# Kernel tuning notes

Measured on AMD Instinct MI355X. Metric: run time of the kernel, lower is better.

The kernel has to match this reference:

```python
import jax, jax.numpy as jnp
import numpy as np

LQ, LK, B, E, H = 1024, 1024, 8, 1024, 16


def setup_inputs() -> dict:
    key0 = jax.random.key(0)
    ks = jax.random.split(key0, 6)
    std = float(np.sqrt(2.0 / (E + E)))
    query = jax.random.normal(ks[0], (LQ, B, E), dtype=jnp.float32)
    key = jax.random.normal(ks[1], (LK, B, E), dtype=jnp.float32)
    attn_mask = jax.random.randint(ks[2], (B, LK), 0, 2).astype(bool)
    in_proj_weight_q = std * jax.random.normal(ks[3], (E, E), dtype=jnp.float32)
    in_proj_weight_kv = std * jax.random.normal(ks[4], (2 * E, E), dtype=jnp.float32)
    out_proj_weight = std * jax.random.normal(ks[5], (E, E), dtype=jnp.float32)
    return {
        "query": query,
        "key": key,
        "attn_mask": attn_mask,
        "in_proj_weight_q": in_proj_weight_q,
        "in_proj_weight_kv": in_proj_weight_kv,
        "out_proj_weight": out_proj_weight,
        "num_heads": H,
    }


def reference(query, key, attn_mask, in_proj_weight_q, in_proj_weight_kv, out_proj_weight, num_heads):
    Lq, Bs, Em = query.shape
    Lk = key.shape[0]
    Hd = Em // num_heads  # head_dim
    scaling = Hd ** (-0.5)

    # input projections: F.linear(x, W) == x @ W.T  (no bias)
    q = jnp.einsum("lbe,fe->lbf", query, in_proj_weight_q) * scaling
    kv = jnp.einsum("lbe,fe->lbf", key, in_proj_weight_kv)
    k, v = jnp.split(kv, 2, axis=-1)

    # [len, b, e] -> [b, h, len, d]
    def to_heads(x, L):
        return x.reshape(L, Bs, num_heads, Hd).transpose(1, 2, 0, 3)

    qh = to_heads(q, Lq)
    kh = to_heads(k, Lk)
    vh = to_heads(v, Lk)

    scores = jnp.einsum("bhqd,bhkd->bhqk", qh, kh)  # [B,H,Lq,Lk]
    neg = jnp.asarray(-1e9, scores.dtype)
    scores = jnp.where(attn_mask[:, None, None, :], neg, scores)
    attn = jax.nn.softmax(scores, axis=-1)  # coverage (dropout=0, eval)

    ctx = jnp.einsum("bhqk,bhkd->bhqd", attn, vh)  # [B,H,Lq,d]
    ctx = ctx.transpose(2, 0, 1, 3).reshape(Lq, Bs, Em)
    out = jnp.einsum("lbe,fe->lbf", ctx, out_proj_weight)
    return out, attn
```

## Files before the change

### kernel.cpp

```cpp
#include <hip/hip_runtime.h>
#include <hip/hip_bf16.h>
#include <cstdint>
#include <cstddef>

constexpr int LQc = 1024, LKc = 1024, Bc = 8, Ec = 1024, Hc = 16, Dc = 64;

typedef __bf16 bf16;
typedef __bf16 bf16x4 __attribute__((ext_vector_type(4)));
typedef __bf16 bf16x8 __attribute__((ext_vector_type(8)));
typedef float  f32x4  __attribute__((ext_vector_type(4)));

#define MFMA16(a, b, c) __builtin_amdgcn_mfma_f32_16x16x32_bf16((a), (b), (c), 0, 0, 0)

__device__ __forceinline__ void gload_lds16(const bf16* g, bf16* l) {
  __builtin_amdgcn_global_load_lds((const __attribute__((address_space(1))) void*)g,
                                   (__attribute__((address_space(3))) void*)l, 16, 0, 0);
}

__global__ __launch_bounds__(256) void k_convert(const float* __restrict__ q,
                                                 const float* __restrict__ k,
                                                 const float* __restrict__ wq,
                                                 const float* __restrict__ wkv,
                                                 const float* __restrict__ wout,
                                                 bf16* __restrict__ dst) {
  const size_t i = ((size_t)blockIdx.x * 256 + threadIdx.x) * 8;
  const float* src; size_t off; float sc = 1.0f;
  if (i < 8388608)        { src = q;    off = i; sc = 0.125f; }
  else if (i < 16777216)  { src = k;    off = i - 8388608; }
  else if (i < 17825792)  { src = wq;   off = i - 16777216; }
  else if (i < 19922944)  { src = wkv;  off = i - 17825792; }
  else                    { src = wout; off = i - 19922944; }
  const f32x4 a = *reinterpret_cast<const f32x4*>(src + off);
  const f32x4 b = *reinterpret_cast<const f32x4*>(src + off + 4);
  bf16x8 o;
  o[0] = (bf16)(a.x * sc); o[1] = (bf16)(a.y * sc);
  o[2] = (bf16)(a.z * sc); o[3] = (bf16)(a.w * sc);
  o[4] = (bf16)(b.x * sc); o[5] = (bf16)(b.y * sc);
  o[6] = (bf16)(b.z * sc); o[7] = (bf16)(b.w * sc);
  *reinterpret_cast<bf16x8*>(dst + i) = o;
}

template <int MODE>
__global__ __launch_bounds__(256) void k_gemm(const bf16* __restrict__ Aq,
                                              const bf16* __restrict__ Ak,
                                              const bf16* __restrict__ Wq,
                                              const bf16* __restrict__ Wkv,
                                              bf16* __restrict__ qh,
                                              bf16* __restrict__ kh,
                                              bf16* __restrict__ vh,
                                              float* __restrict__ o_f) {
  __shared__ bf16 As[128 * 32];
  __shared__ bf16 Bs[128 * 32];

  const int tid  = threadIdx.x;
  const int lane = tid & 63, wave = tid >> 6;
  const int wm = wave & 1, wn = wave >> 1;

  const int cpx = gridDim.x >> 3;
  const int logical = (blockIdx.x & 7) * cpx + (blockIdx.x >> 3);
  const int bx = logical & 63, by = logical >> 6;
  const int m0 = bx * 128;

  const bf16* Ap;
  const bf16* Wp;
  bf16* Op = nullptr;
  if constexpr (MODE == 0) {
    if (by < 8)       { Ap = Aq; Wp = Wq  + (size_t)by * 131072;        Op = qh; }
    else if (by < 16) { Ap = Ak; Wp = Wkv + (size_t)(by - 8) * 131072;  Op = kh; }
    else              { Ap = Ak; Wp = Wkv + 1048576 + (size_t)(by - 16) * 131072; Op = vh; }
  } else {
    Ap = Aq; Wp = Wq + (size_t)by * 131072;
  }
  const int col0 = (by & 7) * 128;

  const int fr = lane & 15, fo = (lane >> 4) * 8;

  f32x4 acc[4][4] = {};

  const int srow = lane >> 2;
  const int scol = (lane & 3) * 8;
  const bf16* ga = Ap + (size_t)(m0 + wave * 32 + srow) * Ec + scol;
  const bf16* gb = Wp + (size_t)(wave * 32 + srow) * Ec + scol;
  bf16* lA = As + wave * 1024;
  bf16* lB = Bs + wave * 1024;

  for (int k0 = 0; k0 < Ec; k0 += 32) {
    gload_lds16(ga + k0, lA);
    gload_lds16(ga + k0 + 16 * Ec, lA + 512);
    gload_lds16(gb + k0, lB);
    gload_lds16(gb + k0 + 16 * Ec, lB + 512);
    __syncthreads();

    bf16x8 a[4], b[4];
#pragma unroll
    for (int i = 0; i < 4; ++i) {
      a[i] = *reinterpret_cast<const bf16x8*>(As + (wm * 64 + i * 16 + fr) * 32 + fo);
      b[i] = *reinterpret_cast<const bf16x8*>(Bs + (wn * 64 + i * 16 + fr) * 32 + fo);
    }
#pragma unroll
    for (int i = 0; i < 4; ++i)
#pragma unroll
      for (int j = 0; j < 4; ++j) acc[i][j] = MFMA16(a[i], b[j], acc[i][j]);
    __syncthreads();
  }

  const int rb = (lane >> 4) * 4;
#pragma unroll
  for (int i = 0; i < 4; ++i) {
#pragma unroll
    for (int j = 0; j < 4; ++j) {
      const int col = col0 + wn * 64 + j * 16 + fr;
#pragma unroll
      for (int r = 0; r < 4; ++r) {
        const int tok = m0 + wm * 64 + i * 16 + rb + r;
        const float val = acc[i][j][r];
        if constexpr (MODE == 0) {
          const int lq = tok >> 3, bb = tok & 7;
          const int h = col >> 6, dd = col & 63;
          Op[(((size_t)(bb * Hc + h)) * LQc + lq) * Dc + dd] = (bf16)val;
        } else {
          o_f[(size_t)tok * Ec + col] = val;
        }
      }
    }
  }
}

__global__ __launch_bounds__(256) void k_vtrans(const bf16* __restrict__ Vh,
                                                bf16* __restrict__ VhT) {
  __shared__ bf16 tile[64][72];
  const int bh = blockIdx.y;
  const int l0 = blockIdx.x * 64;
  const int r = threadIdx.x >> 3, c = (threadIdx.x & 7) * 8;
#pragma unroll
  for (int rr = 0; rr < 2; ++rr) {
    const int row = rr * 32 + r;
    *reinterpret_cast<bf16x8*>(&tile[row][c]) =
        *reinterpret_cast<const bf16x8*>(Vh + ((size_t)bh * LKc + l0 + row) * Dc + c);
  }
  __syncthreads();
#pragma unroll
  for (int rr = 0; rr < 2; ++rr) {
    const int d = rr * 32 + r;
    bf16x8 o;
#pragma unroll
    for (int j = 0; j < 8; ++j) o[j] = tile[c + j][d];
    *reinterpret_cast<bf16x8*>(VhT + ((size_t)bh * Dc + d) * LKc + l0 + c) = o;
  }
}

__global__ __launch_bounds__(256) void k_attn(const bf16* __restrict__ Qh,
                                              const bf16* __restrict__ Kh,
                                              const bf16* __restrict__ VhT,
                                              const int* __restrict__ mask,
                                              float* __restrict__ attn_out,
                                              bf16* __restrict__ ctx_out) {
  __shared__ bf16 sP[32][1032];
  __shared__ float smask[1024];
  __shared__ float psum[4][32];
  __shared__ float rinv[32];

  const int tid = threadIdx.x;
  const int lane = tid & 63, wave = tid >> 6;
  const bool pv_first = (blockIdx.x >> 9) & 1;

  int flat = blockIdx.x;
  flat = (flat & 7) * 512 + (flat >> 3);
  const int bh = flat >> 5;
  const int q0 = (flat & 31) * 32;
  const int b = bh >> 4, h = bh & 15;
  const int fr = lane & 15, fo = (lane >> 4) * 8, rb = (lane >> 4) * 4;

#pragma unroll
  for (int c = tid; c < 1024; c += 256)
    smask[c] = mask[b * LKc + c] ? -1e9f : 0.0f;

  bf16x8 qf[2][2];
  const bf16* Qb = Qh + ((size_t)bh * LQc + q0) * Dc;
#pragma unroll
  for (int m = 0; m < 2; ++m)
#pragma unroll
    for (int kc = 0; kc < 2; ++kc)
      qf[m][kc] = *reinterpret_cast<const bf16x8*>(Qb + (size_t)(m * 16 + fr) * Dc + kc * 32 + fo);
  __syncthreads();

  const bf16* Kb = Kh + (size_t)bh * LKc * Dc;
  float s0[4] = {0.f, 0.f, 0.f, 0.f}, s1[4] = {0.f, 0.f, 0.f, 0.f};
#pragma unroll 4
  for (int t = 0; t < 16; ++t) {
    const int n = (wave * 16 + t) * 16;
    const bf16* kp = Kb + (size_t)(n + fr) * Dc + fo;
    const bf16x8 kf0 = *reinterpret_cast<const bf16x8*>(kp);
    const bf16x8 kf1 = *reinterpret_cast<const bf16x8*>(kp + 32);
    f32x4 c0 = {}, c1 = {};
    c0 = MFMA16(qf[0][0], kf0, c0);
    c0 = MFMA16(qf[0][1], kf1, c0);
    c1 = MFMA16(qf[1][0], kf0, c1);
    c1 = MFMA16(qf[1][1], kf1, c1);
    const int col = n + fr;
    const float madd = smask[col];
#pragma unroll
    for (int r = 0; r < 4; ++r) {
      const float e0 = __expf(c0[r] + madd);
      const float e1 = __expf(c1[r] + madd);
      s0[r] += e0; s1[r] += e1;
      sP[rb + r][col]      = (bf16)e0;
      sP[16 + rb + r][col] = (bf16)e1;
    }
  }
#pragma unroll
  for (int o = 1; o < 16; o <<= 1)
#pragma unroll
    for (int r = 0; r < 4; ++r) {
      s0[r] += __shfl_xor(s0[r], o, 64);
      s1[r] += __shfl_xor(s1[r], o, 64);
    }
  if (fr == 0) {
#pragma unroll
    for (int r = 0; r < 4; ++r) {
      psum[wave][rb + r]      = s0[r];
      psum[wave][16 + rb + r] = s1[r];
    }
  }
  __syncthreads();
  if (tid < 32)
    rinv[tid] = 1.0f / (psum[0][tid] + psum[1][tid] + psum[2][tid] + psum[3][tid]);
  __syncthreads();

  float* ap = attn_out + ((size_t)bh * LQc + q0) * LKc;
  const bf16* Vb = VhT + ((size_t)bh * Dc + wave * 16 + fr) * LKc;
  f32x4 cacc0 = {}, cacc1 = {};

  if (!pv_first) {
#pragma unroll 4
    for (int r = 0; r < 32; ++r) {
      const float rs = rinv[r];
      const bf16x4 v = *reinterpret_cast<const bf16x4*>(&sP[r][tid * 4]);
      f32x4 p;
      p.x = (float)v.x * rs; p.y = (float)v.y * rs;
      p.z = (float)v.z * rs; p.w = (float)v.w * rs;
      __builtin_nontemporal_store(p, reinterpret_cast<f32x4*>(ap + (size_t)r * LKc + tid * 4));
    }
#pragma unroll 4
    for (int kc = 0; kc < 1024; kc += 32) {
      const bf16x8 vf  = *reinterpret_cast<const bf16x8*>(Vb + kc + fo);
      const bf16x8 pa0 = *reinterpret_cast<const bf16x8*>(&sP[fr][kc + fo]);
      const bf16x8 pa1 = *reinterpret_cast<const bf16x8*>(&sP[16 + fr][kc + fo]);
      cacc0 = MFMA16(pa0, vf, cacc0);
      cacc1 = MFMA16(pa1, vf, cacc1);
    }
  } else {
#pragma unroll 4
    for (int kc = 0; kc < 1024; kc += 32) {
      const bf16x8 vf  = *reinterpret_cast<const bf16x8*>(Vb + kc + fo);
      const bf16x8 pa0 = *reinterpret_cast<const bf16x8*>(&sP[fr][kc + fo]);
      const bf16x8 pa1 = *reinterpret_cast<const bf16x8*>(&sP[16 + fr][kc + fo]);
      cacc0 = MFMA16(pa0, vf, cacc0);
      cacc1 = MFMA16(pa1, vf, cacc1);
    }
#pragma unroll 4
    for (int r = 0; r < 32; ++r) {
      const float rs = rinv[r];
      const bf16x4 v = *reinterpret_cast<const bf16x4*>(&sP[r][tid * 4]);
      f32x4 p;
      p.x = (float)v.x * rs; p.y = (float)v.y * rs;
      p.z = (float)v.z * rs; p.w = (float)v.w * rs;
      __builtin_nontemporal_store(p, reinterpret_cast<f32x4*>(ap + (size_t)r * LKc + tid * 4));
    }
  }

  const int e = h * Dc + wave * 16 + fr;
#pragma unroll
  for (int r = 0; r < 4; ++r) {
    const int qa = q0 + rb + r;
    ctx_out[((size_t)qa * Bc + b) * Ec + e] = (bf16)(cacc0[r] * rinv[rb + r]);
    const int qb2 = q0 + 16 + rb + r;
    ctx_out[((size_t)qb2 * Bc + b) * Ec + e] = (bf16)(cacc1[r] * rinv[16 + rb + r]);
  }
}

extern "C" void kernel_launch(void* const* d_in, const int* in_sizes, int n_in,
                              void* d_out, int out_size, void* d_ws, size_t ws_size,
                              hipStream_t stream) {
  const float* query = (const float*)d_in[0];
  const float* keyx  = (const float*)d_in[1];
  const int*   mask  = (const int*)d_in[2];
  const float* wq    = (const float*)d_in[3];
  const float* wkv   = (const float*)d_in[4];
  const float* wout  = (const float*)d_in[5];

  float* out  = (float*)d_out;
  float* attn = out + (size_t)LQc * Bc * Ec;

  bf16* cvt   = (bf16*)d_ws;
  bf16* q2    = cvt;
  bf16* k2    = q2   + 8388608;
  bf16* wqb   = k2   + 8388608;
  bf16* wkvb  = wqb  + 1048576;
  bf16* woutb = wkvb + 2097152;
  bf16* qh    = woutb + 1048576;
  bf16* kh    = qh   + 8388608;
  bf16* vh    = kh   + 8388608;
  bf16* vt    = q2;
  bf16* ctx   = k2;

  k_convert<<<10240, 256, 0, stream>>>(query, keyx, wq, wkv, wout, cvt);
  k_gemm<0><<<1536, 256, 0, stream>>>(q2, k2, wqb, wkvb, qh, kh, vh, nullptr);
  k_vtrans<<<dim3(16, 128), 256, 0, stream>>>(vh, vt);
  k_attn<<<4096, 256, 0, stream>>>(qh, kh, vt, mask, attn, ctx);
  k_gemm<2><<<512, 256, 0, stream>>>(ctx, nullptr, woutb, nullptr, nullptr, nullptr, nullptr, out);
}
```

Baseline: 316.1 us.

## Double attention block size to 512 threads and split PV work across eight waves

Result: slower. 341.0 us (+7.9%).

```diff
diff --git a/kernel.cpp b/kernel.cpp
--- a/kernel.cpp
+++ b/kernel.cpp
@@ -149,15 +149,15 @@
   }
 }
 
-__global__ __launch_bounds__(256) void k_attn(const bf16* __restrict__ Qh,
-                                              const bf16* __restrict__ Kh,
-                                              const bf16* __restrict__ VhT,
-                                              const int* __restrict__ mask,
-                                              float* __restrict__ attn_out,
-                                              bf16* __restrict__ ctx_out) {
+__global__ __launch_bounds__(512, 4) void k_attn(const bf16* __restrict__ Qh,
+                                                 const bf16* __restrict__ Kh,
+                                                 const bf16* __restrict__ VhT,
+                                                 const int* __restrict__ mask,
+                                                 float* __restrict__ attn_out,
+                                                 bf16* __restrict__ ctx_out) {
   __shared__ bf16 sP[32][1032];
   __shared__ float smask[1024];
-  __shared__ float psum[4][32];
+  __shared__ float psum[8][32];
   __shared__ float rinv[32];
 
   const int tid = threadIdx.x;
@@ -171,8 +171,7 @@
   const int b = bh >> 4, h = bh & 15;
   const int fr = lane & 15, fo = (lane >> 4) * 8, rb = (lane >> 4) * 4;
 
-#pragma unroll
-  for (int c = tid; c < 1024; c += 256)
+  for (int c = tid; c < 1024; c += 512)
     smask[c] = mask[b * LKc + c] ? -1e9f : 0.0f;
 
   bf16x8 qf[2][2];
@@ -187,8 +186,8 @@
   const bf16* Kb = Kh + (size_t)bh * LKc * Dc;
   float s0[4] = {0.f, 0.f, 0.f, 0.f}, s1[4] = {0.f, 0.f, 0.f, 0.f};
 #pragma unroll 4
-  for (int t = 0; t < 16; ++t) {
-    const int n = (wave * 16 + t) * 16;
+  for (int t = 0; t < 8; ++t) {
+    const int n = wave * 128 + t * 16;
     const bf16* kp = Kb + (size_t)(n + fr) * Dc + fo;
     const bf16x8 kf0 = *reinterpret_cast<const bf16x8*>(kp);
     const bf16x8 kf1 = *reinterpret_cast<const bf16x8*>(kp + 32);
@@ -223,59 +222,64 @@
     }
   }
   __syncthreads();
-  if (tid < 32)
-    rinv[tid] = 1.0f / (psum[0][tid] + psum[1][tid] + psum[2][tid] + psum[3][tid]);
+  if (tid < 32) {
+    float s = 0.f;
+#pragma unroll
+    for (int w = 0; w < 8; ++w) s += psum[w][tid];
+    rinv[tid] = 1.0f / s;
+  }
   __syncthreads();
 
   float* ap = attn_out + ((size_t)bh * LQc + q0) * LKc;
-  const bf16* Vb = VhT + ((size_t)bh * Dc + wave * 16 + fr) * LKc;
-  f32x4 cacc0 = {}, cacc1 = {};
+  const int mh = wave >> 2, dg = wave & 3;
+  const bf16* Vb = VhT + ((size_t)bh * Dc + dg * 16 + fr) * LKc;
+  f32x4 cacc = {};
+
+  const int wrow = tid >> 8;
+  const int wcol = (tid & 255) * 4;
 
   if (!pv_first) {
 #pragma unroll 4
-    for (int r = 0; r < 32; ++r) {
+    for (int it = 0; it < 16; ++it) {
+      const int r = it * 2 + wrow;
       const float rs = rinv[r];
-      const bf16x4 v = *reinterpret_cast<const bf16x4*>(&sP[r][tid * 4]);
+      const bf16x4 v = *reinterpret_cast<const bf16x4*>(&sP[r][wcol]);
       f32x4 p;
       p.x = (float)v.x * rs; p.y = (float)v.y * rs;
       p.z = (float)v.z * rs; p.w = (float)v.w * rs;
-      __builtin_nontemporal_store(p, reinterpret_cast<f32x4*>(ap + (size_t)r * LKc + tid * 4));
+      __builtin_nontemporal_store(p, reinterpret_cast<f32x4*>(ap + (size_t)r * LKc + wcol));
     }
 #pragma unroll 4
     for (int kc = 0; kc < 1024; kc += 32) {
-      const bf16x8 vf  = *reinterpret_cast<const bf16x8*>(Vb + kc + fo);
-      const bf16x8 pa0 = *reinterpret_cast<const bf16x8*>(&sP[fr][kc + fo]);
-      const bf16x8 pa1 = *reinterpret_cast<const bf16x8*>(&sP[16 + fr][kc + fo]);
-      cacc0 = MFMA16(pa0, vf, cacc0);
-      cacc1 = MFMA16(pa1, vf, cacc1);
+      const bf16x8 vf = *reinterpret_cast<const bf16x8*>(Vb + kc + fo);
+      const bf16x8 pa = *reinterpret_cast<const bf16x8*>(&sP[mh * 16 + fr][kc + fo]);
+      cacc = MFMA16(pa, vf, cacc);
     }
   } else {
 #pragma unroll 4
     for (int kc = 0; kc < 1024; kc += 32) {
-      const bf16x8 vf  = *reinterpret_cast<const bf16x8*>(Vb + kc + fo);
-      const bf16x8 pa0 = *reinterpret_cast<const bf16x8*>(&sP[fr][kc + fo]);
-      const bf16x8 pa1 = *reinterpret_cast<const bf16x8*>(&sP[16 + fr][kc + fo]);
-      cacc0 = MFMA16(pa0, vf, cacc0);
-      cacc1 = MFMA16(pa1, vf, cacc1);
-    }
-#pragma unroll 4
-    for (int r = 0; r < 32; ++r) {
+      const bf16x8 vf = *reinterpret_cast<const bf16x8*>(Vb + kc + fo);
+      const bf16x8 pa = *reinterpret_cast<const bf16x8*>(&sP[mh * 16 + fr][kc + fo]);
+      cacc = MFMA16(pa, vf, cacc);
+    }
+#pragma unroll 4
+    for (int it = 0; it < 16; ++it) {
+      const int r = it * 2 + wrow;
       const float rs = rinv[r];
-      const bf16x4 v = *reinterpret_cast<const bf16x4*>(&sP[r][tid * 4]);
+      const bf16x4 v = *reinterpret_cast<const bf16x4*>(&sP[r][wcol]);
       f32x4 p;
       p.x = (float)v.x * rs; p.y = (float)v.y * rs;
       p.z = (float)v.z * rs; p.w = (float)v.w * rs;
-      __builtin_nontemporal_store(p, reinterpret_cast<f32x4*>(ap + (size_t)r * LKc + tid * 4));
-    }
-  }
-
-  const int e = h * Dc + wave * 16 + fr;
+      __builtin_nontemporal_store(p, reinterpret_cast<f32x4*>(ap + (size_t)r * LKc + wcol));
+    }
+  }
+
+  const int e = h * Dc + dg * 16 + fr;
 #pragma unroll
   for (int r = 0; r < 4; ++r) {
-    const int qa = q0 + rb + r;
-    ctx_out[((size_t)qa * Bc + b) * Ec + e] = (bf16)(cacc0[r] * rinv[rb + r]);
-    const int qb2 = q0 + 16 + rb + r;
-    ctx_out[((size_t)qb2 * Bc + b) * Ec + e] = (bf16)(cacc1[r] * rinv[16 + rb + r]);
+    const int row = mh * 16 + rb + r;
+    const int qa = q0 + row;
+    ctx_out[((size_t)qa * Bc + b) * Ec + e] = (bf16)(cacc[r] * rinv[row]);
   }
 }
 
@@ -307,6 +311,6 @@
   k_convert<<<10240, 256, 0, stream>>>(query, keyx, wq, wkv, wout, cvt);
   k_gemm<0><<<1536, 256, 0, stream>>>(q2, k2, wqb, wkvb, qh, kh, vh, nullptr);
   k_vtrans<<<dim3(16, 128), 256, 0, stream>>>(vh, vt);
-  k_attn<<<4096, 256, 0, stream>>>(qh, kh, vt, mask, attn, ctx);
+  k_attn<<<4096, 512, 0, stream>>>(qh, kh, vt, mask, attn, ctx);
   k_gemm<2><<<512, 256, 0, stream>>>(ctx, nullptr, woutb, nullptr, nullptr, nullptr, nullptr, out);
 }
```

## Fuse V transpose into projection GEMM epilogue via LDS staging

Applied to the files above, without the earlier changes.

Result: slower. 328.3 us (+3.9%).

```diff
diff --git a/kernel.cpp b/kernel.cpp
--- a/kernel.cpp
+++ b/kernel.cpp
@@ -49,8 +49,9 @@
                                               bf16* __restrict__ kh,
                                               bf16* __restrict__ vh,
                                               float* __restrict__ o_f) {
-  __shared__ bf16 As[128 * 32];
-  __shared__ bf16 Bs[128 * 32];
+  __shared__ bf16 smem[9216];
+  bf16* As = smem;
+  bf16* Bs = smem + 4096;
 
   const int tid  = threadIdx.x;
   const int lane = tid & 63, wave = tid >> 6;
@@ -105,47 +106,69 @@
   }
 
   const int rb = (lane >> 4) * 4;
-#pragma unroll
-  for (int i = 0; i < 4; ++i) {
-#pragma unroll
-    for (int j = 0; j < 4; ++j) {
-      const int col = col0 + wn * 64 + j * 16 + fr;
-#pragma unroll
-      for (int r = 0; r < 4; ++r) {
-        const int tok = m0 + wm * 64 + i * 16 + rb + r;
-        const float val = acc[i][j][r];
-        if constexpr (MODE == 0) {
-          const int lq = tok >> 3, bb = tok & 7;
-          const int h = col >> 6, dd = col & 63;
-          Op[(((size_t)(bb * Hc + h)) * LQc + lq) * Dc + dd] = (bf16)val;
-        } else {
-          o_f[(size_t)tok * Ec + col] = val;
+
+  if constexpr (MODE == 0) {
+    if (by < 16) {
+#pragma unroll
+      for (int i = 0; i < 4; ++i) {
+#pragma unroll
+        for (int j = 0; j < 4; ++j) {
+          const int col = col0 + wn * 64 + j * 16 + fr;
+#pragma unroll
+          for (int r = 0; r < 4; ++r) {
+            const int tok = m0 + wm * 64 + i * 16 + rb + r;
+            const int lq = tok >> 3, bb = tok & 7;
+            const int h = col >> 6, dd = col & 63;
+            Op[(((size_t)(bb * Hc + h)) * LQc + lq) * Dc + dd] = (bf16)acc[i][j][r];
+          }
         }
       }
-    }
-  }
-}
-
-__global__ __launch_bounds__(256) void k_vtrans(const bf16* __restrict__ Vh,
-                                                bf16* __restrict__ VhT) {
-  __shared__ bf16 tile[64][72];
-  const int bh = blockIdx.y;
-  const int l0 = blockIdx.x * 64;
-  const int r = threadIdx.x >> 3, c = (threadIdx.x & 7) * 8;
-#pragma unroll
-  for (int rr = 0; rr < 2; ++rr) {
-    const int row = rr * 32 + r;
-    *reinterpret_cast<bf16x8*>(&tile[row][c]) =
-        *reinterpret_cast<const bf16x8*>(Vh + ((size_t)bh * LKc + l0 + row) * Dc + c);
-  }
-  __syncthreads();
-#pragma unroll
-  for (int rr = 0; rr < 2; ++rr) {
-    const int d = rr * 32 + r;
-    bf16x8 o;
-#pragma unroll
-    for (int j = 0; j < 8; ++j) o[j] = tile[c + j][d];
-    *reinterpret_cast<bf16x8*>(VhT + ((size_t)bh * Dc + d) * LKc + l0 + c) = o;
+    } else {
+      const int hbase = (by - 16) * 2;
+      const int lk0 = m0 >> 3;
+      for (int chunk = 0; chunk < 2; ++chunk) {
+        __syncthreads();
+        if (wn == chunk) {
+#pragma unroll
+          for (int i = 0; i < 4; ++i)
+#pragma unroll
+            for (int j = 0; j < 4; ++j)
+#pragma unroll
+              for (int r = 0; r < 4; ++r)
+                smem[(wm * 64 + i * 16 + rb + r) * 72 + j * 16 + fr] =
+                    (bf16)acc[i][j][r];
+        }
+        __syncthreads();
+        const int h = hbase + chunk;
+#pragma unroll
+        for (int pp = 0; pp < 2; ++pp) {
+          const int p = tid * 2 + pp;
+          const int fl = p >> 3, bb = p & 7;
+          bf16x8 o0, o1;
+#pragma unroll
+          for (int k = 0; k < 8; ++k) {
+            o0[k] = smem[(bb + k * 8) * 72 + fl];
+            o1[k] = smem[(bb + (k + 8) * 8) * 72 + fl];
+          }
+          bf16* dst = Op + (((size_t)(bb * Hc + h)) * Dc + fl) * LKc + lk0;
+          *reinterpret_cast<bf16x8*>(dst) = o0;
+          *reinterpret_cast<bf16x8*>(dst + 8) = o1;
+        }
+      }
+    }
+  } else {
+#pragma unroll
+    for (int i = 0; i < 4; ++i) {
+#pragma unroll
+      for (int j = 0; j < 4; ++j) {
+        const int col = col0 + wn * 64 + j * 16 + fr;
+#pragma unroll
+        for (int r = 0; r < 4; ++r) {
+          const int tok = m0 + wm * 64 + i * 16 + rb + r;
+          o_f[(size_t)tok * Ec + col] = acc[i][j][r];
+        }
+      }
+    }
   }
 }
 
@@ -300,13 +323,11 @@
   bf16* woutb = wkvb + 2097152;
   bf16* qh    = woutb + 1048576;
   bf16* kh    = qh   + 8388608;
-  bf16* vh    = kh   + 8388608;
-  bf16* vt    = q2;
+  bf16* vt    = kh   + 8388608;
   bf16* ctx   = k2;
 
   k_convert<<<10240, 256, 0, stream>>>(query, keyx, wq, wkv, wout, cvt);
-  k_gemm<0><<<1536, 256, 0, stream>>>(q2, k2, wqb, wkvb, qh, kh, vh, nullptr);
-  k_vtrans<<<dim3(16, 128), 256, 0, stream>>>(vh, vt);
+  k_gemm<0><<<1536, 256, 0, stream>>>(q2, k2, wqb, wkvb, qh, kh, vt, nullptr);
   k_attn<<<4096, 256, 0, stream>>>(qh, kh, vt, mask, attn, ctx);
   k_gemm<2><<<512, 256, 0, stream>>>(ctx, nullptr, woutb, nullptr, nullptr, nullptr, nullptr, out);
 }
```
